# Kernel tuning notes

Hardware: AMD Instinct MI355X
Metric: run time of the kernel (lower is better)

The kernel has to match this reference:

```python
import math
import jax, jax.numpy as jnp
from jax import lax
import numpy as np

RADIUS = 6
K = 2 * RADIUS + 1  # 13


def _conv(x, w, b, stride):
    # torch Conv2d(kernel=3, padding=1)
    y = lax.conv_general_dilated(
        x, w, window_strides=(stride, stride), padding=((1, 1), (1, 1)),
        dimension_numbers=("NCHW", "OIHW", "NCHW"))
    return y + b[None, :, None, None]


def _encoder(x, w1, b1, w2, b2, w3, b3):
    x = jax.nn.relu(_conv(x, w1, b1, 1))
    x = jax.nn.relu(_conv(x, w2, b2, 2))
    x = jax.nn.relu(_conv(x, w3, b3, 2))
    return x  # [B,128,H/4,W/4]


def _local_corr(z_t, z_t1):
    # Equivalent to unfold(z_t1, K, pad=RADIUS) -> multiply z_t -> sum over C,
    # but computed per-offset to avoid materializing [B,C,K*K,H,W].
    B, C, H, W = z_t.shape
    zp = jnp.pad(z_t1, ((0, 0), (0, 0), (RADIUS, RADIUS), (RADIUS, RADIUS)))
    inv_sqrt_c = 1.0 / np.sqrt(C).astype(np.float32)
    # unfold flattening order is (ki, kj) row-major, matching this loop order
    slabs = [
        (z_t * zp[:, :, i:i + H, j:j + W]).sum(axis=1)
        for i in range(K) for j in range(K)
    ]
    return jnp.stack(slabs, axis=1) * inv_sqrt_c  # [B, K*K, H, W]


def setup_inputs() -> dict:
    key = jax.random.key(0)
    ks = jax.random.split(key, 10)
    f32 = jnp.float32

    def w_init(k, shape, fan_in):
        return jax.random.normal(k, shape, dtype=f32) * np.sqrt(2.0 / fan_in).astype(np.float32)

    return {
        "img_t": jax.random.normal(ks[0], (32, 3, 256, 256), dtype=f32),
        "img_t1": jax.random.normal(ks[1], (32, 3, 256, 256), dtype=f32),
        "w1": w_init(ks[2], (32, 3, 3, 3), 3 * 9),
        "b1": jnp.zeros((32,), dtype=f32),
        "w2": w_init(ks[3], (64, 32, 3, 3), 32 * 9),
        "b2": jnp.zeros((64,), dtype=f32),
        "w3": w_init(ks[4], (128, 64, 3, 3), 64 * 9),
        "b3": jnp.zeros((128,), dtype=f32),
        "w_head": w_init(ks[5], (2, K * K), K * K),
        "b_head": jnp.zeros((2,), dtype=f32),
    }


def reference(img_t, img_t1, w1, b1, w2, b2, w3, b3, w_head, b_head):
    z_t = _encoder(img_t, w1, b1, w2, b2, w3, b3)
    z_t1 = _encoder(img_t1, w1, b1, w2, b2, w3, b3)
    corr = _local_corr(z_t, z_t1)          # [B, 169, H/4, W/4]
    h_t = corr.mean(axis=(2, 3))           # [B, 169]
    pred = h_t @ w_head.T + b_head         # [B, 2]
    return (pred, z_t, z_t1, corr, h_t)
```

## Files before the change

kernel.cpp:

```cpp
#include <hip/hip_runtime.h>

typedef _Float16 f16;
typedef _Float16 h4 __attribute__((ext_vector_type(4)));
typedef _Float16 v8h __attribute__((ext_vector_type(8)));
typedef _Float16 h8 __attribute__((ext_vector_type(8)));
typedef float v4f __attribute__((ext_vector_type(4)));

#define INV_SQRT_C 0.08838834764831845f

__global__ void wt1_k(const float* __restrict__ w1, f16* __restrict__ wT)
{
  int idx = blockIdx.x * 256 + threadIdx.x;
  int k = idx & 31, row = idx >> 5;
  float v = 0.f;
  if (row < 32) {
    int oc = row, q = k >> 3, j = k & 7;
    if (q < 3) v = w1[(oc * 3 + q) * 9 + j];
  } else {
    int oc = row - 32;
    if (k < 3) v = w1[(oc * 3 + k) * 9 + 8];
  }
  wT[idx] = (f16)v;
}

__global__ void wt2_k(const float* __restrict__ w2, f16* __restrict__ wT)
{
  int idx = blockIdx.x * 256 + threadIdx.x;
  int ic = idx & 31, oc = (idx >> 5) & 63, khkw = idx >> 11;
  wT[idx] = (f16)w2[(oc * 32 + ic) * 9 + khkw];
}

__global__ void wt3_k(const float* __restrict__ w3, f16* __restrict__ wT)
{
  int idx = blockIdx.x * 256 + threadIdx.x;
  int ic5 = idx & 31, oc = (idx >> 5) & 127, ch = idx >> 12;
  int khkw = ch >> 1, ich = ch & 1;
  int ic = ich * 32 + ic5;
  wT[idx] = (f16)w3[(oc * 64 + ic) * 9 + khkw];
}

#define STAGE_ISSUE(OH)                                                     \
  {                                                                         \
    int ihb_ = 2 * (OH) - 2;                                                \
    _Pragma("unroll")                                                       \
    for (int i = 0; i < 3; i++) {                                           \
      int ih = ihb_ + rS[i], iw = ibase + colS[i];                          \
      bool ok = pokS[i] && ((unsigned)ih < 256u) && ((unsigned)iw < 256u);  \
      const float* rp = imgb + ih * 256 + iw;                               \
      g0[i] = ok ? rp[0] : 0.f;                                             \
      g1[i] = ok ? rp[65536] : 0.f;                                         \
      g2[i] = ok ? rp[131072] : 0.f;                                        \
    }                                                                       \
  }

#define STAGE_WRITE(BUF)                                                    \
  {                                                                         \
    _Pragma("unroll")                                                       \
    for (int i = 0; i < 3; i++) {                                           \
      if (pokS[i]) {                                                        \
        h4 pk;                                                              \
        pk[0] = (f16)g0[i]; pk[1] = (f16)g1[i];                             \
        pk[2] = (f16)g2[i]; pk[3] = (f16)0.f;                               \
        *(h4*)(&sImgF[BUF][rS[i]][colS[i]][0]) = pk;                        \
      }                                                                     \
    }                                                                       \
  }

__global__ __launch_bounds__(256, 4) void conv12_m(const float* __restrict__ img_t,
    const float* __restrict__ img_t1,
    const f16* __restrict__ wT1, const float* __restrict__ b1,
    const f16* __restrict__ wT2, const float* __restrict__ b2, f16* __restrict__ out)
{
  const int ohc = blockIdx.x, g = blockIdx.y, bb = blockIdx.z;
  const int tid = threadIdx.x;
  const int lane = tid & 63, wv = tid >> 6;
  const int n15 = lane & 15, quad = lane >> 4;

  __shared__ f16 sImgF[2][5][134][4];
  __shared__ f16 sA[3 * 132 * 40];

  const int OW0 = g * 64;
  const int ibase = 2 * OW0 - 2;
  const float* imgb = (bb < 32 ? img_t : img_t1) + (long)(bb & 31) * 3 * 65536;

  int colS[3], rS[3]; bool pokS[3];
  #pragma unroll
  for (int i = 0; i < 3; i++) {
    int p = tid + i * 256;
    pokS[i] = p < 670;
    int pc = pokS[i] ? p : 0;
    colS[i] = pc % 134; rS[i] = pc / 134;
  }

  v8h a0 = *(const v8h*)(wT1 + n15 * 32 + quad * 8);
  v8h a1 = *(const v8h*)(wT1 + (16 + n15) * 32 + quad * 8);
  v8h a2 = *(const v8h*)(wT1 + (32 + n15) * 32 + quad * 8);
  v8h a3 = *(const v8h*)(wT1 + (48 + n15) * 32 + quad * 8);
  float4 bb0 = *(const float4*)(b1 + quad * 4);
  float4 bb1 = *(const float4*)(b1 + 16 + quad * 4);

  float g0[3], g1[3], g2[3];
  const int oh0 = ohc * 8;

  STAGE_ISSUE(oh0);
  STAGE_WRITE(0);

  for (int it = 0; it < 8; it++) {
    const int oh = oh0 + it;
    const int cur = it & 1;
    if (it < 7) STAGE_ISSUE(oh + 1);
    __syncthreads();

    for (int grp = wv; grp < 25; grp += 4) {
      int p = grp * 16 + n15;
      bool pv = p < 387;
      int pc = pv ? p : 386;
      int yr = pc >= 258 ? 2 : (pc >= 129 ? 1 : 0);
      int ci = pc - yr * 129;
      const f16* sp = &sImgF[cur][yr][ci][0] + quad;
      v8h B1;
      #pragma unroll
      for (int j = 0; j < 8; j++)
        B1[j] = sp[(j / 3) * 536 + (j % 3) * 4];
      h4 t = *(const h4*)(&sImgF[cur][yr + 2][ci + 2][0]);
      v8h B2;
      B2[0] = t[0]; B2[1] = t[1]; B2[2] = t[2]; B2[3] = t[3];
      B2[4] = t[0]; B2[5] = t[1]; B2[6] = t[2]; B2[7] = t[3];
      v4f acc0 = {}, acc1 = {};
      acc0 = __builtin_amdgcn_mfma_f32_16x16x32_f16(a0, B1, acc0, 0, 0, 0);
      acc1 = __builtin_amdgcn_mfma_f32_16x16x32_f16(a1, B1, acc1, 0, 0, 0);
      acc0 = __builtin_amdgcn_mfma_f32_16x16x32_f16(a2, B2, acc0, 0, 0, 0);
      acc1 = __builtin_amdgcn_mfma_f32_16x16x32_f16(a3, B2, acc1, 0, 0, 0);
      int y = 2 * oh - 1 + yr;
      int iw = ibase + 1 + ci;
      bool valid = pv && ((unsigned)y < 256u) && ((unsigned)iw < 256u);
      f16* base = &sA[(yr * 132 + ci) * 40];
      h4 pk0, pk1;
      #pragma unroll
      for (int r = 0; r < 4; r++) {
        float v0 = acc0[r] + ((const float*)&bb0)[r];
        float v1 = acc1[r] + ((const float*)&bb1)[r];
        pk0[r] = (f16)((valid && v0 > 0.f) ? v0 : 0.f);
        pk1[r] = (f16)((valid && v1 > 0.f) ? v1 : 0.f);
      }
      if (pv) {
        *(h4*)(base + quad * 4) = pk0;
        *(h4*)(base + 16 + quad * 4) = pk1;
      }
    }
    __syncthreads();

    v4f acc[4] = {};
    for (int kh = 0; kh < 3; kh++) {
      for (int kw = 0; kw < 3; kw++) {
        int khkw = kh * 3 + kw;
        const f16* wp = wT2 + khkw * 2048 + n15 * 32 + quad * 8;
        v8h w0 = *(const v8h*)(wp);
        v8h w1v = *(const v8h*)(wp + 512);
        v8h w2v = *(const v8h*)(wp + 1024);
        v8h w3v = *(const v8h*)(wp + 1536);
        int ci = 32 * wv + 2 * n15 + kw;
        v8h bf = *(const v8h*)&sA[(kh * 132 + ci) * 40 + quad * 8];
        acc[0] = __builtin_amdgcn_mfma_f32_16x16x32_f16(w0, bf, acc[0], 0, 0, 0);
        acc[1] = __builtin_amdgcn_mfma_f32_16x16x32_f16(w1v, bf, acc[1], 0, 0, 0);
        acc[2] = __builtin_amdgcn_mfma_f32_16x16x32_f16(w2v, bf, acc[2], 0, 0, 0);
        acc[3] = __builtin_amdgcn_mfma_f32_16x16x32_f16(w3v, bf, acc[3], 0, 0, 0);
      }
    }
    const int ow = OW0 + wv * 16 + n15;
    #pragma unroll
    for (int mt = 0; mt < 4; mt++) {
      int oc0 = mt * 16 + quad * 4;
      float4 bbv = *(const float4*)(b2 + oc0);
      h4 pk;
      #pragma unroll
      for (int r = 0; r < 4; r++) {
        float v = acc[mt][r] + ((const float*)&bbv)[r];
        pk[r] = (f16)(v > 0.f ? v : 0.f);
      }
      *(h4*)(out + (((long)(bb * 128 + oh) * 128 + ow) * 64) + oc0) = pk;
    }

    if (it < 7) STAGE_WRITE(cur ^ 1);
  }
}

__global__ __launch_bounds__(256, 3) void conv3_m(const f16* __restrict__ in,
    const f16* __restrict__ wT, const float* __restrict__ b3,
    float* __restrict__ zbase, f16* __restrict__ nhbase)
{
  const int oh = blockIdx.x, bb = blockIdx.y;
  const int ib = bb >> 5, b = bb & 31;
  const int tid = threadIdx.x;
  const int lane = tid & 63, wv = tid >> 6;
  const int n15 = lane & 15, quad = lane >> 4;
  const int ow = wv * 16 + n15;

  __shared__ f16 sIn[3 * 128 * 64];

  const f16* inb = in + (long)bb * (128 * 128 * 64);
  const int ih0 = 2 * oh - 1;

  {
    h8 stg[12];
    #pragma unroll
    for (int i = 0; i < 12; i++) {
      int idx = tid + i * 256;
      int ck = idx & 7, iw = (idx >> 3) & 127, r = idx >> 10;
      int ih = ih0 + r;
      h8 v;
      #pragma unroll
      for (int e = 0; e < 8; e++) v[e] = (f16)0.f;
      if ((unsigned)ih < 128u) v = *(const h8*)(inb + ((long)(ih * 128 + iw)) * 64 + ck * 8);
      stg[i] = v;
    }
    #pragma unroll
    for (int i = 0; i < 12; i++) {
      int idx = tid + i * 256;
      int ck = idx & 7, iw = (idx >> 3) & 127, r = idx >> 10;
      int sck = ck ^ ((iw >> 1) & 7);
      *(h8*)(&sIn[(r * 128 + iw) * 64 + sck * 8]) = stg[i];
    }
  }
  __syncthreads();

  v4f acc[8] = {};
  for (int kh = 0; kh < 3; kh++) {
    for (int kw = 0; kw < 3; kw++) {
      int iw = 2 * ow + kw - 1;
      bool bok = (unsigned)iw < 128u;
      int iwc = bok ? iw : 0;
      #pragma unroll
      for (int ich = 0; ich < 2; ich++) {
        int ch = (kh * 3 + kw) * 2 + ich;
        int ck = ich * 4 + quad;
        int sck = ck ^ ((iwc >> 1) & 7);
        v8h bf;
        #pragma unroll
        for (int e = 0; e < 8; e++) bf[e] = (f16)0.f;
        if (bok) bf = *(const v8h*)&sIn[(kh * 128 + iwc) * 64 + sck * 8];
        const f16* wp = wT + ((long)(ch * 128 + n15)) * 32 + quad * 8;
        #pragma unroll
        for (int mt = 0; mt < 8; mt++) {
          v8h a = *(const v8h*)(wp + mt * 512);
          acc[mt] = __builtin_amdgcn_mfma_f32_16x16x32_f16(a, bf, acc[mt], 0, 0, 0);
        }
      }
    }
  }

  float* zo = zbase + (long)ib * 16777216L;
  f16* nh = nhbase + (long)ib * 16777216L;
  #pragma unroll
  for (int mt = 0; mt < 8; mt++) {
    int oc0 = mt * 16 + quad * 4;
    float4 bbv = *(const float4*)(b3 + oc0);
    float rv[4];
    #pragma unroll
    for (int r = 0; r < 4; r++) {
      float v = acc[mt][r] + ((const float*)&bbv)[r];
      rv[r] = v > 0.f ? v : 0.f;
    }
    #pragma unroll
    for (int r = 0; r < 4; r++)
      zo[(((long)(b * 128 + oc0 + r) * 64 + oh) * 64) + ow] = rv[r];
    h4 pk;
    #pragma unroll
    for (int r = 0; r < 4; r++) pk[r] = (f16)rv[r];
    *(h4*)(nh + (((long)(b * 64 + oh) * 64 + ow) * 128) + oc0) = pk;
  }
}

__global__ __launch_bounds__(256) void corr_m(const f16* __restrict__ zt,
    const f16* __restrict__ zt1, float* __restrict__ corr, float* __restrict__ part)
{
  const int h = blockIdx.x, b = blockIdx.y;
  const int lane = threadIdx.x & 63, wv = threadIdx.x >> 6;
  const int n15 = lane & 15, quad = lane >> 4;
  const int w0 = wv * 16;
  __shared__ float sC[64][17];

  const f16* arow = zt + (((long)(b * 64 + h) * 64 + (w0 + n15)) * 128) + quad * 8;
  v8h A[4];
  #pragma unroll
  for (int ks = 0; ks < 4; ks++) A[ks] = *(const v8h*)(arow + ks * 32);

  float* cb = corr + (long)b * 169 * 4096 + h * 64;

  const int q4r0 = quad * 4;
  const int wq0 = w0 - 6 + n15;
  const int wq1 = w0 + 10 + n15;
  const bool ok0 = (unsigned)wq0 < 64u;
  const bool ok1 = (unsigned)wq1 < 64u;

  for (int ki = 0; ki < 13; ki++) {
    int row = h + ki - 6;
    bool rok = (unsigned)row < 64u;
    v4f acc0 = {}, acc1 = {};
    if (rok) {
      const f16* brow = zt1 + ((long)(b * 64 + row) * 64) * 128;
      const f16* bp0 = brow + (long)wq0 * 128 + quad * 8;
      const f16* bp1 = brow + (long)wq1 * 128 + quad * 8;
      #pragma unroll
      for (int ks = 0; ks < 4; ks++) {
        v8h b0, b1;
        #pragma unroll
        for (int k = 0; k < 8; k++) { b0[k] = (f16)0.f; b1[k] = (f16)0.f; }
        if (ok0) b0 = *(const v8h*)(bp0 + ks * 32);
        if (ok1) b1 = *(const v8h*)(bp1 + ks * 32);
        acc0 = __builtin_amdgcn_mfma_f32_16x16x32_f16(A[ks], b0, acc0, 0, 0, 0);
        acc1 = __builtin_amdgcn_mfma_f32_16x16x32_f16(A[ks], b1, acc1, 0, 0, 0);
      }
    }
    __syncthreads();
    #pragma unroll
    for (int r = 0; r < 4; r++) {
      int q4r = q4r0 + r;
      int w = w0 + q4r;
      int kj0 = n15 - q4r;
      if (kj0 >= 0 && kj0 < 13) sC[w][kj0] = acc0[r] * INV_SQRT_C;
      int kj1 = kj0 + 16;
      if (kj1 < 13) sC[w][kj1] = acc1[r] * INV_SQRT_C;
    }
    __syncthreads();
    for (int idx = threadIdx.x; idx < 832; idx += 256) {
      int w = idx & 63, kj = idx >> 6;
      float v = sC[w][kj];
      cb[(long)(ki * 13 + kj) * 4096 + w] = v;
      #pragma unroll
      for (int off = 32; off > 0; off >>= 1) v += __shfl_down(v, off, 64);
      if (lane == 0) part[(long)(ki * 13 + kj) * 2048 + b * 64 + h] = v;
    }
  }
}

__global__ __launch_bounds__(256) void ht2_k(const float* __restrict__ part,
                                             float* __restrict__ ht)
{
  int o = blockIdx.x;
  int t = threadIdx.x;
  int b = t >> 3, s = t & 7;
  const float* p = part + (long)o * 2048 + b * 64 + s * 8;
  float v = 0.f;
  #pragma unroll
  for (int i = 0; i < 8; i++) v += p[i];
  #pragma unroll
  for (int off = 4; off > 0; off >>= 1) v += __shfl_down(v, off, 8);
  if (s == 0) ht[b * 169 + o] = v * (1.f / 4096.f);
}

__global__ void pred_k(const float* __restrict__ ht, const float* __restrict__ wh,
                       const float* __restrict__ bh, float* __restrict__ pred)
{
  int t = threadIdx.x;
  int b = t >> 1, j = t & 1;
  float s = bh[j];
  for (int o = 0; o < 169; o++) s = fmaf(ht[b * 169 + o], wh[j * 169 + o], s);
  pred[b * 2 + j] = s;
}

extern "C" void kernel_launch(void* const* d_in, const int* in_sizes, int n_in,
                              void* d_out, int out_size, void* d_ws, size_t ws_size,
                              hipStream_t stream)
{
  (void)in_sizes; (void)n_in; (void)out_size; (void)ws_size;
  const float* img_t  = (const float*)d_in[0];
  const float* img_t1 = (const float*)d_in[1];
  const float* w1 = (const float*)d_in[2];
  const float* b1 = (const float*)d_in[3];
  const float* w2 = (const float*)d_in[4];
  const float* b2 = (const float*)d_in[5];
  const float* w3 = (const float*)d_in[6];
  const float* b3 = (const float*)d_in[7];
  const float* wh = (const float*)d_in[8];
  const float* bh = (const float*)d_in[9];
  float* out = (float*)d_out;

  char* ws = (char*)d_ws;
  f16* bufB = (f16*)ws;
  f16* nhT  = (f16*)(ws + 134217728L);
  float* part = (float*)(ws + 201326592L);

  const long OUT_ZT   = 64;
  const long OUT_ZT1  = OUT_ZT + 16777216L;
  const long OUT_CORR = OUT_ZT1 + 16777216L;
  const long OUT_HT   = OUT_CORR + 22151168L;

  f16* wT1 = (f16*)(out + OUT_CORR);
  f16* wT2 = wT1 + 2048;
  f16* wT3 = wT2 + 18432;

  wt1_k<<<8, 256, 0, stream>>>(w1, wT1);
  wt2_k<<<72, 256, 0, stream>>>(w2, wT2);
  wt3_k<<<288, 256, 0, stream>>>(w3, wT3);

  conv12_m<<<dim3(16, 2, 64), 256, 0, stream>>>(img_t, img_t1, wT1, b1, wT2, b2, bufB);
  conv3_m<<<dim3(64, 64), 256, 0, stream>>>(bufB, wT3, b3, out + OUT_ZT, nhT);
  corr_m<<<dim3(64, 32), 256, 0, stream>>>(nhT, nhT + 16777216L, out + OUT_CORR, part);
  ht2_k<<<169, 256, 0, stream>>>(part, out + OUT_HT);
  pred_k<<<1, 64, 0, stream>>>(out + OUT_HT, wh, bh, out);
}
```

Baseline: 681.3 us.

## Restructure conv3 into persistent row-chunk blocks with LDS weights and prefetched slabs

Each conv3 block now computes 16 output rows for half of the output channels. It stages that half of the weights once into LDS (padded rows), and double-buffers the next input slab through registers while the MFMAs run on the current row. Before, every block handled one row and all 128 channels and read weights from global memory each time. The change is meant to cut repeated global weight traffic and hide slab load latency. In exchange it uses far more LDS per block, which lowers occupancy (launch bounds 1), and the grid shrinks to 512 blocks, re-reading each input slab once per channel group.

```diff
diff --git a/kernel.cpp b/kernel.cpp
--- a/kernel.cpp
+++ b/kernel.cpp
@@ -185,89 +185,129 @@
   }
 }
 
-__global__ __launch_bounds__(256, 3) void conv3_m(const f16* __restrict__ in,
+#define ISSUE_SLAB(OH)                                                         \
+  {                                                                            \
+    int ih0_ = 2 * (OH) - 1;                                                   \
+    _Pragma("unroll")                                                          \
+    for (int i = 0; i < 12; i++) {                                             \
+      int ih = ih0_ + rS3[i];                                                  \
+      h8 v;                                                                    \
+      _Pragma("unroll")                                                        \
+      for (int e = 0; e < 8; e++) v[e] = (f16)0.f;                             \
+      if ((unsigned)ih < 128u)                                                 \
+        v = *(const h8*)(inb + ((long)(ih * 128 + iwS3[i])) * 64 + ckS3[i] * 8); \
+      stg[i] = v;                                                              \
+    }                                                                          \
+  }
+
+#define WRITE_SLAB()                                                           \
+  {                                                                            \
+    _Pragma("unroll")                                                          \
+    for (int i = 0; i < 12; i++)                                               \
+      *(h8*)(&sIn[(rS3[i] * 128 + iwS3[i]) * 64 + sckS3[i] * 8]) = stg[i];     \
+  }
+
+__global__ __launch_bounds__(256, 1) void conv3_m(const f16* __restrict__ in,
     const f16* __restrict__ wT, const float* __restrict__ b3,
     float* __restrict__ zbase, f16* __restrict__ nhbase)
 {
-  const int oh = blockIdx.x, bb = blockIdx.y;
+  const int ohc = blockIdx.x, bb = blockIdx.y, ocg = blockIdx.z;
   const int ib = bb >> 5, b = bb & 31;
   const int tid = threadIdx.x;
   const int lane = tid & 63, wv = tid >> 6;
   const int n15 = lane & 15, quad = lane >> 4;
   const int ow = wv * 16 + n15;
 
+  __shared__ f16 sW[18 * 64 * 40];
   __shared__ f16 sIn[3 * 128 * 64];
 
   const f16* inb = in + (long)bb * (128 * 128 * 64);
-  const int ih0 = 2 * oh - 1;
-
-  {
-    h8 stg[12];
-    #pragma unroll
-    for (int i = 0; i < 12; i++) {
-      int idx = tid + i * 256;
-      int ck = idx & 7, iw = (idx >> 3) & 127, r = idx >> 10;
-      int ih = ih0 + r;
-      h8 v;
-      #pragma unroll
-      for (int e = 0; e < 8; e++) v[e] = (f16)0.f;
-      if ((unsigned)ih < 128u) v = *(const h8*)(inb + ((long)(ih * 128 + iw)) * 64 + ck * 8);
-      stg[i] = v;
-    }
-    #pragma unroll
-    for (int i = 0; i < 12; i++) {
-      int idx = tid + i * 256;
-      int ck = idx & 7, iw = (idx >> 3) & 127, r = idx >> 10;
-      int sck = ck ^ ((iw >> 1) & 7);
-      *(h8*)(&sIn[(r * 128 + iw) * 64 + sck * 8]) = stg[i];
-    }
-  }
+
+  int ckS3[12], iwS3[12], rS3[12], sckS3[12];
+  #pragma unroll
+  for (int i = 0; i < 12; i++) {
+    int idx = tid + i * 256;
+    ckS3[i] = idx & 7; iwS3[i] = (idx >> 3) & 127; rS3[i] = idx >> 10;
+    sckS3[i] = ckS3[i] ^ ((iwS3[i] >> 1) & 7);
+  }
+
+  h8 wstg[18];
+  #pragma unroll
+  for (int i = 0; i < 18; i++) {
+    int idx = tid + i * 256;
+    int kc = idx & 3, oc = (idx >> 2) & 63, ch = idx >> 8;
+    wstg[i] = *(const h8*)(wT + ((long)(ch * 128 + ocg * 64 + oc) << 5) + kc * 8);
+  }
+  const int oh0 = ohc * 16;
+  h8 stg[12];
+  ISSUE_SLAB(oh0);
+  #pragma unroll
+  for (int i = 0; i < 18; i++) {
+    int idx = tid + i * 256;
+    int kc = idx & 3, oc = (idx >> 2) & 63, ch = idx >> 8;
+    *(h8*)(&sW[(ch * 64 + oc) * 40 + kc * 8]) = wstg[i];
+  }
+  WRITE_SLAB();
   __syncthreads();
 
-  v4f acc[8] = {};
-  for (int kh = 0; kh < 3; kh++) {
-    for (int kw = 0; kw < 3; kw++) {
-      int iw = 2 * ow + kw - 1;
-      bool bok = (unsigned)iw < 128u;
-      int iwc = bok ? iw : 0;
-      #pragma unroll
-      for (int ich = 0; ich < 2; ich++) {
-        int ch = (kh * 3 + kw) * 2 + ich;
-        int ck = ich * 4 + quad;
-        int sck = ck ^ ((iwc >> 1) & 7);
-        v8h bf;
-        #pragma unroll
-        for (int e = 0; e < 8; e++) bf[e] = (f16)0.f;
-        if (bok) bf = *(const v8h*)&sIn[(kh * 128 + iwc) * 64 + sck * 8];
-        const f16* wp = wT + ((long)(ch * 128 + n15)) * 32 + quad * 8;
-        #pragma unroll
-        for (int mt = 0; mt < 8; mt++) {
-          v8h a = *(const v8h*)(wp + mt * 512);
-          acc[mt] = __builtin_amdgcn_mfma_f32_16x16x32_f16(a, bf, acc[mt], 0, 0, 0);
-        }
-      }
-    }
-  }
-
+  const f16* swb = sW + n15 * 40 + quad * 8;
   float* zo = zbase + (long)ib * 16777216L;
   f16* nh = nhbase + (long)ib * 16777216L;
-  #pragma unroll
-  for (int mt = 0; mt < 8; mt++) {
-    int oc0 = mt * 16 + quad * 4;
-    float4 bbv = *(const float4*)(b3 + oc0);
-    float rv[4];
+
+  for (int it = 0; it < 16; it++) {
+    const int oh = oh0 + it;
+    if (it < 15) ISSUE_SLAB(oh + 1);
+
+    v4f acc[4] = {};
+    for (int kh = 0; kh < 3; kh++) {
+      #pragma unroll
+      for (int kw = 0; kw < 3; kw++) {
+        int iw = 2 * ow + kw - 1;
+        bool bok = (unsigned)iw < 128u;
+        int iwc = bok ? iw : 0;
+        #pragma unroll
+        for (int ich = 0; ich < 2; ich++) {
+          int ch = (kh * 3 + kw) * 2 + ich;
+          int ck = ich * 4 + quad;
+          int sck = ck ^ ((iwc >> 1) & 7);
+          v8h bf;
+          #pragma unroll
+          for (int e = 0; e < 8; e++) bf[e] = (f16)0.f;
+          if (bok) bf = *(const v8h*)&sIn[(kh * 128 + iwc) * 64 + sck * 8];
+          const f16* wp = swb + ch * (64 * 40);
+          #pragma unroll
+          for (int mt = 0; mt < 4; mt++) {
+            v8h a = *(const v8h*)(wp + mt * (16 * 40));
+            acc[mt] = __builtin_amdgcn_mfma_f32_16x16x32_f16(a, bf, acc[mt], 0, 0, 0);
+          }
+        }
+      }
+    }
+
     #pragma unroll
-    for (int r = 0; r < 4; r++) {
-      float v = acc[mt][r] + ((const float*)&bbv)[r];
-      rv[r] = v > 0.f ? v : 0.f;
-    }
-    #pragma unroll
-    for (int r = 0; r < 4; r++)
-      zo[(((long)(b * 128 + oc0 + r) * 64 + oh) * 64) + ow] = rv[r];
-    h4 pk;
-    #pragma unroll
-    for (int r = 0; r < 4; r++) pk[r] = (f16)rv[r];
-    *(h4*)(nh + (((long)(b * 64 + oh) * 64 + ow) * 128) + oc0) = pk;
+    for (int mt = 0; mt < 4; mt++) {
+      int oc0 = ocg * 64 + mt * 16 + quad * 4;
+      float4 bbv = *(const float4*)(b3 + oc0);
+      float rv[4];
+      #pragma unroll
+      for (int r = 0; r < 4; r++) {
+        float v = acc[mt][r] + ((const float*)&bbv)[r];
+        rv[r] = v > 0.f ? v : 0.f;
+      }
+      #pragma unroll
+      for (int r = 0; r < 4; r++)
+        zo[(((long)(b * 128 + oc0 + r) * 64 + oh) * 64) + ow] = rv[r];
+      h4 pk;
+      #pragma unroll
+      for (int r = 0; r < 4; r++) pk[r] = (f16)rv[r];
+      *(h4*)(nh + (((long)(b * 64 + oh) * 64 + ow) * 128) + oc0) = pk;
+    }
+
+    __syncthreads();
+    if (it < 15) {
+      WRITE_SLAB();
+      __syncthreads();
+    }
   }
 }
 
@@ -395,7 +435,7 @@
   wt3_k<<<288, 256, 0, stream>>>(w3, wT3);
 
   conv12_m<<<dim3(16, 2, 64), 256, 0, stream>>>(img_t, img_t1, wT1, b1, wT2, b2, bufB);
-  conv3_m<<<dim3(64, 64), 256, 0, stream>>>(bufB, wT3, b3, out + OUT_ZT, nhT);
+  conv3_m<<<dim3(4, 64, 2), 256, 0, stream>>>(bufB, wT3, b3, out + OUT_ZT, nhT);
   corr_m<<<dim3(64, 32), 256, 0, stream>>>(nhT, nhT + 16777216L, out + OUT_CORR, part);
   ht2_k<<<169, 256, 0, stream>>>(part, out + OUT_HT);
   pred_k<<<1, 64, 0, stream>>>(out + OUT_HT, wh, bh, out);
```

After: 600.3 us. 11.9% less time.
